# Kernel optimization log

Hardware: AMD Instinct MI355X
Metric: run time of the kernel (lower is better)

The kernel has to match this reference:

```python
import jax, jax.numpy as jnp
import numpy as np

B, S, D, H, FACTOR = 1, 2048, 1024, 16, 16
HD = D // H


def setup_inputs() -> dict:
    key = jax.random.key(0)
    ks = jax.random.split(key, 9)
    s = 1.0 / np.sqrt(D)
    u = lambda k, shape: jax.random.uniform(k, shape, jnp.float32, -s, s)
    return {
        "x": jax.random.normal(ks[0], (B, S, D), jnp.float32),
        "Wq": u(ks[1], (D, D)), "bq": u(ks[2], (D,)),
        "Wk": u(ks[3], (D, D)), "bk": u(ks[4], (D,)),
        "Wv": u(ks[5], (D, D)), "bv": u(ks[6], (D,)),
        "Wo": u(ks[7], (D, D)), "bo": u(ks[8], (D,)),
    }


def reference(x, Wq, bq, Wk, bk, Wv, bv, Wo, bo):
    b, s, d = x.shape
    h, hd = H, HD
    # projections -> [b, h, s, hd]
    q = (x @ Wq + bq).reshape(b, s, h, hd).transpose(0, 2, 1, 3)
    k = (x @ Wk + bk).reshape(b, s, h, hd).transpose(0, 2, 1, 3)
    v = (x @ Wv + bv).reshape(b, s, h, hd).transpose(0, 2, 1, 3)
    # dense scores [b, h, s, s]
    scores = jnp.einsum('bhqd,bhkd->bhqk', q, k) / np.sqrt(hd).astype(np.float32)
    # top-k along last dim, scatter into zeros (non-topk entries stay 0, as in torch code)
    vals, idx = jax.lax.top_k(scores, FACTOR)  # [b,h,s,FACTOR]
    flat_scores = scores.reshape(-1, s)
    rows = jnp.arange(flat_scores.shape[0])[:, None]
    sparse = jnp.zeros_like(flat_scores).at[rows, idx.reshape(-1, FACTOR)].set(
        vals.reshape(-1, FACTOR)).reshape(scores.shape)
    attn = jax.nn.softmax(sparse, axis=-1)  # softmax over sparse scores incl. zeros
    out = jnp.einsum('bhqk,bhkd->bhqd', attn, v)
    out = out.transpose(0, 2, 1, 3).reshape(b, s, d)
    return out @ Wo + bo
```

## Files before the change

kernel.cpp:

```cpp
#include <hip/hip_runtime.h>
#include <stdint.h>

constexpr int SEQ  = 2048;
constexpr int DIM  = 1024;
constexpr int NH   = 16;
constexpr int HDIM = 64;
constexpr int TOPK = 16;
constexpr int CAP  = 96;
constexpr int CST  = 97;
constexpr int QR   = 32;

typedef unsigned short bf16_t;
typedef __attribute__((ext_vector_type(8))) short bf16x8;
typedef __attribute__((ext_vector_type(4))) float f32x4;
typedef unsigned long long u64;

__device__ __forceinline__ int swzc(int col, int row) { return col ^ ((row & 7) << 3); }

__device__ __forceinline__ float bf2f(bf16_t b) {
  return __uint_as_float(((unsigned)b) << 16);
}
__device__ __forceinline__ bf16_t f2bf(float f) {
  unsigned u = __float_as_uint(f);
  unsigned r = u + 0x7fffu + ((u >> 16) & 1u);
  return (bf16_t)(r >> 16);
}
__device__ __forceinline__ f32x4 zero4() {
  f32x4 z; z[0] = 0.f; z[1] = 0.f; z[2] = 0.f; z[3] = 0.f; return z;
}
__device__ __forceinline__ void gload_lds16(const bf16_t* g, bf16_t* l) {
  __builtin_amdgcn_global_load_lds(
      (const __attribute__((address_space(1))) void*)g,
      (__attribute__((address_space(3))) void*)l, 16, 0, 0);
}
__device__ __forceinline__ unsigned ordf(float f) {
  unsigned b = __float_as_uint(f);
  return (b & 0x80000000u) ? ~b : (b | 0x80000000u);
}
__device__ __forceinline__ float iordf(unsigned u) {
  unsigned b = (u & 0x80000000u) ? (u ^ 0x80000000u) : ~u;
  return __uint_as_float(b);
}

__global__ void prep_kernel(const float* __restrict__ x, bf16_t* __restrict__ xb,
                            const float* __restrict__ W0, const float* __restrict__ W1,
                            const float* __restrict__ W2, const float* __restrict__ W3,
                            bf16_t* __restrict__ T0, bf16_t* __restrict__ T1,
                            bf16_t* __restrict__ T2, bf16_t* __restrict__ T3) {
  const int z = blockIdx.z;
  if (z == 4) {
    int bl = blockIdx.y * 32 + blockIdx.x;
    int tt = threadIdx.y * 32 + threadIdx.x;
    int i = (bl * 256 + tt) * 8;
    float4 v0 = *reinterpret_cast<const float4*>(x + i);
    float4 v1 = *reinterpret_cast<const float4*>(x + i + 4);
    bf16x8 o;
    o[0] = (short)f2bf(v0.x); o[1] = (short)f2bf(v0.y);
    o[2] = (short)f2bf(v0.z); o[3] = (short)f2bf(v0.w);
    o[4] = (short)f2bf(v1.x); o[5] = (short)f2bf(v1.y);
    o[6] = (short)f2bf(v1.z); o[7] = (short)f2bf(v1.w);
    *reinterpret_cast<bf16x8*>(xb + i) = o;
    return;
  }
  const float* W = (z == 0) ? W0 : (z == 1) ? W1 : (z == 2) ? W2 : W3;
  bf16_t* WT = (z == 0) ? T0 : (z == 1) ? T1 : (z == 2) ? T2 : T3;
  __shared__ float tile[32][33];
  int tx = threadIdx.x, ty = threadIdx.y;
  int bx = blockIdx.x * 32, by = blockIdx.y * 32;
#pragma unroll
  for (int i = 0; i < 4; ++i)
    tile[ty + i * 8][tx] = W[(by + ty + i * 8) * DIM + bx + tx];
  __syncthreads();
#pragma unroll
  for (int i = 0; i < 4; ++i)
    WT[(bx + ty + i * 8) * DIM + by + tx] = f2bf(tile[tx][ty + i * 8]);
}

template <int MODE>
__global__ __launch_bounds__(256) void gemm_t(const bf16_t* __restrict__ A,
                                              const bf16_t* __restrict__ B0,
                                              const bf16_t* __restrict__ B1,
                                              const bf16_t* __restrict__ B2,
                                              const float* __restrict__ c0,
                                              const float* __restrict__ c1,
                                              const float* __restrict__ c2,
                                              void* __restrict__ o0,
                                              void* __restrict__ o1,
                                              void* __restrict__ o2,
                                              float* __restrict__ sumv) {
  __shared__ __align__(16) bf16_t As[2][128 * 64];
  __shared__ __align__(16) bf16_t Bs[2][128 * 64];
  const int t = threadIdx.x;
  int which, bn0, ks0, nst;
  if (MODE == 0) {
    which = blockIdx.x >> 3; bn0 = (blockIdx.x & 7) * 128; ks0 = 0; nst = 16;
  } else {
    which = 0; bn0 = blockIdx.x * 128; ks0 = blockIdx.z * 8; nst = 8;
  }
  const bf16_t* Bt = (which == 0) ? B0 : (which == 1) ? B1 : B2;
  const float* bias = (which == 0) ? c0 : (which == 1) ? c1 : c2;
  void* out = (which == 0) ? o0 : (which == 1) ? o1 : o2;
  const int bm0 = blockIdx.y * 128;
  const int w = t >> 6, lane = t & 63, lr = lane & 15, lg = lane >> 4;
  const int wm = w >> 1, wn = w & 1;
  const int srow = t >> 3;
  const int scol = swzc((t & 7) * 8, srow);
  const int ldst = srow * 64 + (t & 7) * 8;
  const int rsw = (lr & 7) << 3;

  f32x4 acc[4][4];
#pragma unroll
  for (int m = 0; m < 4; ++m)
#pragma unroll
    for (int n = 0; n < 4; ++n) acc[m][n] = zero4();

#define STAGE_G(buf, kt)                                                             \
  do {                                                                               \
    _Pragma("unroll") for (int i_ = 0; i_ < 4; ++i_) {                               \
      gload_lds16(A + (size_t)(bm0 + i_ * 32 + srow) * DIM + (kt) * 64 + scol,       \
                  &As[buf][i_ * 32 * 64 + ldst]);                                    \
      gload_lds16(Bt + (size_t)(bn0 + i_ * 32 + srow) * DIM + (kt) * 64 + scol,      \
                  &Bs[buf][i_ * 32 * 64 + ldst]);                                    \
    }                                                                                \
  } while (0)

  STAGE_G(0, ks0);
  __syncthreads();

  for (int s = 0; s < nst; ++s) {
    const int cur = s & 1;
    if (s < nst - 1) STAGE_G(cur ^ 1, ks0 + s + 1);
    bf16x8 a[4][2], b[4][2];
#pragma unroll
    for (int m = 0; m < 4; ++m)
#pragma unroll
      for (int kk = 0; kk < 2; ++kk)
        a[m][kk] = *reinterpret_cast<const bf16x8*>(
            &As[cur][(wm * 64 + m * 16 + lr) * 64 + ((kk * 32 + lg * 8) ^ rsw)]);
#pragma unroll
    for (int n = 0; n < 4; ++n)
#pragma unroll
      for (int kk = 0; kk < 2; ++kk)
        b[n][kk] = *reinterpret_cast<const bf16x8*>(
            &Bs[cur][(wn * 64 + n * 16 + lr) * 64 + ((kk * 32 + lg * 8) ^ rsw)]);
#pragma unroll
    for (int m = 0; m < 4; ++m)
#pragma unroll
      for (int n = 0; n < 4; ++n)
#pragma unroll
        for (int kk = 0; kk < 2; ++kk)
          acc[m][n] = __builtin_amdgcn_mfma_f32_16x16x32_bf16(a[m][kk], b[n][kk],
                                                              acc[m][n], 0, 0, 0);
    __syncthreads();
  }
#undef STAGE_G

#pragma unroll
  for (int n = 0; n < 4; ++n) {
    int col = bn0 + wn * 64 + n * 16 + lr;
    float bv = bias[col];
    if (MODE == 0) {
      float colsum = 0.f;
#pragma unroll
      for (int m = 0; m < 4; ++m)
#pragma unroll
        for (int r = 0; r < 4; ++r) {
          int row = bm0 + wm * 64 + m * 16 + lg * 4 + r;
          bf16_t rb = f2bf(acc[m][n][r] + bv);
          reinterpret_cast<bf16_t*>(out)[(size_t)row * DIM + col] = rb;
          if (which == 2) colsum += bf2f(rb);
        }
      if (which == 2) atomicAdd(&sumv[col], colsum);
    } else {
      float badd = (ks0 == 0) ? bv : 0.f;
#pragma unroll
      for (int m = 0; m < 4; ++m)
#pragma unroll
        for (int r = 0; r < 4; ++r) {
          int row = bm0 + wm * 64 + m * 16 + lg * 4 + r;
          atomicAdd(reinterpret_cast<float*>(out) + (size_t)row * DIM + col,
                    acc[m][n][r] + badd);
        }
    }
  }
}

#define LOADK(buf, kc)                                                              \
  do {                                                                              \
    _Pragma("unroll") for (int n_ = 0; n_ < 4; ++n_)                                \
      _Pragma("unroll") for (int k_ = 0; k_ < 2; ++k_)                              \
        kf[buf][n_][k_] = *reinterpret_cast<const bf16x8*>(                         \
            kp + (size_t)((kc) * 64 + n_ * 16 + lr) * DIM + k_ * 32 + lg * 8);      \
  } while (0)

__global__ __launch_bounds__(256, 4) void attn_kernel(const bf16_t* __restrict__ q,
                                                      const bf16_t* __restrict__ k,
                                                      const bf16_t* __restrict__ v,
                                                      const float* __restrict__ sumv,
                                                      bf16_t* __restrict__ op) {
  __shared__ float CM[QR * 33];
  __shared__ float Tsh[QR];
  __shared__ float zsh[QR];
  __shared__ int   cnt[QR];
  __shared__ float cval[QR * CST];
  __shared__ unsigned short cidx[QR * CST];

  const int t = threadIdx.x;
  const int lin = blockIdx.x;
  const int xcd = lin & 7, ixd = lin >> 3;
  const int h = xcd * 2 + (ixd >> 6), qt = ixd & 63;
  const int w = t >> 6, lane = t & 63, lr = lane & 15, lg = lane >> 4;

  const bf16_t* qp = q + (size_t)(qt * QR) * DIM + h * HDIM;
  const bf16_t* kp = k + h * HDIM;

  bf16x8 aq[2][2];
#pragma unroll
  for (int m = 0; m < 2; ++m)
#pragma unroll
    for (int kk = 0; kk < 2; ++kk)
      aq[m][kk] = *reinterpret_cast<const bf16x8*>(
          qp + (size_t)(m * 16 + lr) * DIM + kk * 32 + lg * 8);

  bf16x8 kf[2][4][2];

  LOADK(0, w * 8);
#pragma unroll
  for (int i = 0; i < 8; ++i) {
    if (i < 7) LOADK((i + 1) & 1, w * 8 + i + 1);
    const int cur = i & 1;
    f32x4 sacc[2][4];
#pragma unroll
    for (int m = 0; m < 2; ++m)
#pragma unroll
      for (int n = 0; n < 4; ++n) sacc[m][n] = zero4();
#pragma unroll
    for (int m = 0; m < 2; ++m)
#pragma unroll
      for (int n = 0; n < 4; ++n)
#pragma unroll
        for (int kk = 0; kk < 2; ++kk)
          sacc[m][n] = __builtin_amdgcn_mfma_f32_16x16x32_bf16(kf[cur][n][kk], aq[m][kk],
                                                               sacc[m][n], 0, 0, 0);
#pragma unroll
    for (int m = 0; m < 2; ++m) {
      float mx = sacc[m][0][0];
#pragma unroll
      for (int n = 0; n < 4; ++n)
#pragma unroll
        for (int r = 0; r < 4; ++r) mx = fmaxf(mx, sacc[m][n][r]);
      mx = fmaxf(mx, __shfl_xor(mx, 16));
      mx = fmaxf(mx, __shfl_xor(mx, 32));
      if (lane < 16) CM[(m * 16 + lane) * 33 + (w * 8 + i)] = mx * 0.125f;
    }
  }
  LOADK(0, w * 8);
  __syncthreads();

  {
    const int trow = t >> 3, tsub = t & 7;
    float cmv[4];
#pragma unroll
    for (int c = 0; c < 4; ++c) cmv[c] = CM[trow * 33 + tsub * 4 + c];
    float Tval = -1e30f;
#pragma unroll
    for (int it = 0; it < TOPK; ++it) {
      float lm = fmaxf(fmaxf(cmv[0], cmv[1]), fmaxf(cmv[2], cmv[3]));
      float gm = fmaxf(lm, __shfl_xor(lm, 1));
      gm = fmaxf(gm, __shfl_xor(gm, 2));
      gm = fmaxf(gm, __shfl_xor(gm, 4));
      u64 b = __ballot(lm == gm);
      int base = lane & ~7;
      int ownsub = __ffsll((b >> base) & 0xFFull) - 1;
      if (tsub == ownsub) {
        bool d = false;
#pragma unroll
        for (int c = 0; c < 4; ++c)
          if (!d && cmv[c] == lm) { cmv[c] = -1e30f; d = true; }
      }
      Tval = gm;
    }
    if (tsub == 0) { Tsh[trow] = Tval; cnt[trow] = 0; }
  }
  __syncthreads();

  float Treg[2];
#pragma unroll
  for (int m = 0; m < 2; ++m) Treg[m] = Tsh[m * 16 + lr];

#pragma unroll
  for (int i = 0; i < 8; ++i) {
    if (i < 7) LOADK((i + 1) & 1, w * 8 + i + 1);
    const int cur = i & 1;
    const int kc = w * 8 + i;
    f32x4 sacc[2][4];
#pragma unroll
    for (int m = 0; m < 2; ++m)
#pragma unroll
      for (int n = 0; n < 4; ++n) sacc[m][n] = zero4();
#pragma unroll
    for (int m = 0; m < 2; ++m)
#pragma unroll
      for (int n = 0; n < 4; ++n)
#pragma unroll
        for (int kk = 0; kk < 2; ++kk)
          sacc[m][n] = __builtin_amdgcn_mfma_f32_16x16x32_bf16(kf[cur][n][kk], aq[m][kk],
                                                               sacc[m][n], 0, 0, 0);
#pragma unroll
    for (int m = 0; m < 2; ++m)
#pragma unroll
      for (int n = 0; n < 4; ++n)
#pragma unroll
        for (int r = 0; r < 4; ++r) {
          float val = sacc[m][n][r] * 0.125f;
          if (val >= Treg[m]) {
            int row = m * 16 + lr;
            int p = atomicAdd(&cnt[row], 1);
            if (p < CAP) {
              cval[row * CST + p] = val;
              cidx[row * CST + p] = (unsigned short)(kc * 64 + n * 16 + lg * 4 + r);
            }
          }
        }
  }
  __syncthreads();

  {
    const int trow = t >> 3, tsub = t & 7;
    int nc = cnt[trow]; if (nc > CAP) nc = CAP;
    float Zexp = 0.f;
    for (int sel = 0; sel < TOPK; ++sel) {
      u64 lmax = 0ull; int lp = -1;
      for (int p = tsub; p < nc; p += 8) {
        float vv = cval[trow * CST + p];
        unsigned id = cidx[trow * CST + p];
        u64 key = ((u64)ordf(vv) << 32) | (u64)(unsigned)(~id);
        if (key > lmax) { lmax = key; lp = p; }
      }
      u64 g = lmax;
#pragma unroll
      for (int d = 1; d < 8; d <<= 1) {
        u64 o = __shfl_xor(g, d);
        g = (o > g) ? o : g;
      }
      if (lmax == g && lp >= 0) cval[trow * CST + lp] = -1e30f;
      float val = iordf((unsigned)(g >> 32));
      int idx = (int)(~(unsigned)(g & 0xffffffffull));
      float e = expf(val);
      Zexp += e;
      if (tsub == 0) {
        CM[trow * 33 + sel] = e - 1.f;
        CM[trow * 33 + 16 + sel] = __int_as_float(idx);
      }
    }
    if (tsub == 0) zsh[trow] = 2032.f + Zexp;
  }
  __syncthreads();

  {
    const int row = t >> 3;
    const int dbase = h * HDIM + (t & 7) * 8;
    float oacc[8];
    const float4* sp = reinterpret_cast<const float4*>(sumv + dbase);
    float4 s0 = sp[0], s1 = sp[1];
    oacc[0] = s0.x; oacc[1] = s0.y; oacc[2] = s0.z; oacc[3] = s0.w;
    oacc[4] = s1.x; oacc[5] = s1.y; oacc[6] = s1.z; oacc[7] = s1.w;
    float invZ = 1.f / zsh[row];
#pragma unroll
    for (int j = 0; j < TOPK; ++j) {
      float wj = CM[row * 33 + j];
      int kidx = __float_as_int(CM[row * 33 + 16 + j]);
      bf16x8 vv = *reinterpret_cast<const bf16x8*>(v + (size_t)kidx * DIM + dbase);
#pragma unroll
      for (int e = 0; e < 8; ++e) oacc[e] += wj * bf2f((bf16_t)vv[e]);
    }
    bf16x8 o0;
#pragma unroll
    for (int e = 0; e < 8; ++e) o0[e] = (short)f2bf(oacc[e] * invZ);
    *reinterpret_cast<bf16x8*>(op + (size_t)(qt * QR + row) * DIM + dbase) = o0;
  }
}

extern "C" void kernel_launch(void* const* d_in, const int* in_sizes, int n_in,
                              void* d_out, int out_size, void* d_ws, size_t ws_size,
                              hipStream_t stream) {
  const float* x  = (const float*)d_in[0];
  const float* Wq = (const float*)d_in[1];
  const float* bq = (const float*)d_in[2];
  const float* Wk = (const float*)d_in[3];
  const float* bk = (const float*)d_in[4];
  const float* Wv = (const float*)d_in[5];
  const float* bv = (const float*)d_in[6];
  const float* Wo = (const float*)d_in[7];
  const float* bo = (const float*)d_in[8];
  float* out = (float*)d_out;

  char* ws = (char*)d_ws;
  bf16_t* xb   = (bf16_t*)(ws + (size_t)(0)  * (1 << 20));
  bf16_t* WqT  = (bf16_t*)(ws + (size_t)(4)  * (1 << 20));
  bf16_t* WkT  = (bf16_t*)(ws + (size_t)(6)  * (1 << 20));
  bf16_t* WvT  = (bf16_t*)(ws + (size_t)(8)  * (1 << 20));
  bf16_t* WoT  = (bf16_t*)(ws + (size_t)(10) * (1 << 20));
  bf16_t* qb   = (bf16_t*)(ws + (size_t)(12) * (1 << 20));
  bf16_t* kb   = (bf16_t*)(ws + (size_t)(16) * (1 << 20));
  bf16_t* vb   = (bf16_t*)(ws + (size_t)(20) * (1 << 20));
  bf16_t* opb  = (bf16_t*)(ws + (size_t)(24) * (1 << 20));
  float*  sumv = (float*) (ws + (size_t)(28) * (1 << 20));

  prep_kernel<<<dim3(32, 32, 5), dim3(32, 8), 0, stream>>>(x, xb, Wq, Wk, Wv, Wo,
                                                           WqT, WkT, WvT, WoT);
  hipMemsetAsync(sumv, 0, DIM * sizeof(float), stream);
  hipMemsetAsync(out, 0, (size_t)SEQ * DIM * sizeof(float), stream);

  gemm_t<0><<<dim3(24, 16), 256, 0, stream>>>(xb, WqT, WkT, WvT, bq, bk, bv,
                                              (void*)qb, (void*)kb, (void*)vb, sumv);

  attn_kernel<<<1024, 256, 0, stream>>>(qb, kb, vb, sumv, opb);

  gemm_t<1><<<dim3(8, 16, 2), 256, 0, stream>>>(opb, WoT, WoT, WoT, bo, bo, bo,
                                                (void*)out, (void*)out, (void*)out, sumv);
}
```

Before: 255.3 us.

## Replace split-K atomic output GEMM with 128x64 tiled direct-store kernel

The output projection GEMM drops its split-K layout, which relied on float atomicAdd into a zeroed output. It now uses a dedicated kernel with 128x64 tiles and a 16x16 grid that covers the full K dimension and stores results directly, so the output memset and the atomics go away. The attention kernel's launch bounds change from 4 to 2 waves-per-EU minimum, which allows more registers but may lower occupancy. Each block now does more K iterations, and there are 256 blocks instead of the earlier 256 split-K blocks.

```diff
diff --git a/kernel.cpp b/kernel.cpp
--- a/kernel.cpp
+++ b/kernel.cpp
@@ -76,31 +76,25 @@
     WT[(bx + ty + i * 8) * DIM + by + tx] = f2bf(tile[tx][ty + i * 8]);
 }
 
-template <int MODE>
-__global__ __launch_bounds__(256) void gemm_t(const bf16_t* __restrict__ A,
-                                              const bf16_t* __restrict__ B0,
-                                              const bf16_t* __restrict__ B1,
-                                              const bf16_t* __restrict__ B2,
-                                              const float* __restrict__ c0,
-                                              const float* __restrict__ c1,
-                                              const float* __restrict__ c2,
-                                              void* __restrict__ o0,
-                                              void* __restrict__ o1,
-                                              void* __restrict__ o2,
-                                              float* __restrict__ sumv) {
+__global__ __launch_bounds__(256) void gemm_qkv(const bf16_t* __restrict__ A,
+                                                const bf16_t* __restrict__ B0,
+                                                const bf16_t* __restrict__ B1,
+                                                const bf16_t* __restrict__ B2,
+                                                const float* __restrict__ c0,
+                                                const float* __restrict__ c1,
+                                                const float* __restrict__ c2,
+                                                bf16_t* __restrict__ o0,
+                                                bf16_t* __restrict__ o1,
+                                                bf16_t* __restrict__ o2,
+                                                float* __restrict__ sumv) {
   __shared__ __align__(16) bf16_t As[2][128 * 64];
   __shared__ __align__(16) bf16_t Bs[2][128 * 64];
   const int t = threadIdx.x;
-  int which, bn0, ks0, nst;
-  if (MODE == 0) {
-    which = blockIdx.x >> 3; bn0 = (blockIdx.x & 7) * 128; ks0 = 0; nst = 16;
-  } else {
-    which = 0; bn0 = blockIdx.x * 128; ks0 = blockIdx.z * 8; nst = 8;
-  }
+  const int which = blockIdx.x >> 3;
   const bf16_t* Bt = (which == 0) ? B0 : (which == 1) ? B1 : B2;
   const float* bias = (which == 0) ? c0 : (which == 1) ? c1 : c2;
-  void* out = (which == 0) ? o0 : (which == 1) ? o1 : o2;
-  const int bm0 = blockIdx.y * 128;
+  bf16_t* out = (which == 0) ? o0 : (which == 1) ? o1 : o2;
+  const int bm0 = blockIdx.y * 128, bn0 = (blockIdx.x & 7) * 128;
   const int w = t >> 6, lane = t & 63, lr = lane & 15, lg = lane >> 4;
   const int wm = w >> 1, wn = w & 1;
   const int srow = t >> 3;
@@ -124,12 +118,12 @@
     }                                                                                \
   } while (0)
 
-  STAGE_G(0, ks0);
-  __syncthreads();
-
-  for (int s = 0; s < nst; ++s) {
+  STAGE_G(0, 0);
+  __syncthreads();
+
+  for (int s = 0; s < 16; ++s) {
     const int cur = s & 1;
-    if (s < nst - 1) STAGE_G(cur ^ 1, ks0 + s + 1);
+    if (s < 15) STAGE_G(cur ^ 1, s + 1);
     bf16x8 a[4][2], b[4][2];
 #pragma unroll
     for (int m = 0; m < 4; ++m)
@@ -159,29 +153,93 @@
   for (int n = 0; n < 4; ++n) {
     int col = bn0 + wn * 64 + n * 16 + lr;
     float bv = bias[col];
-    if (MODE == 0) {
-      float colsum = 0.f;
-#pragma unroll
-      for (int m = 0; m < 4; ++m)
-#pragma unroll
-        for (int r = 0; r < 4; ++r) {
-          int row = bm0 + wm * 64 + m * 16 + lg * 4 + r;
-          bf16_t rb = f2bf(acc[m][n][r] + bv);
-          reinterpret_cast<bf16_t*>(out)[(size_t)row * DIM + col] = rb;
-          if (which == 2) colsum += bf2f(rb);
-        }
-      if (which == 2) atomicAdd(&sumv[col], colsum);
-    } else {
-      float badd = (ks0 == 0) ? bv : 0.f;
-#pragma unroll
-      for (int m = 0; m < 4; ++m)
-#pragma unroll
-        for (int r = 0; r < 4; ++r) {
-          int row = bm0 + wm * 64 + m * 16 + lg * 4 + r;
-          atomicAdd(reinterpret_cast<float*>(out) + (size_t)row * DIM + col,
-                    acc[m][n][r] + badd);
-        }
-    }
+    float colsum = 0.f;
+#pragma unroll
+    for (int m = 0; m < 4; ++m)
+#pragma unroll
+      for (int r = 0; r < 4; ++r) {
+        int row = bm0 + wm * 64 + m * 16 + lg * 4 + r;
+        bf16_t rb = f2bf(acc[m][n][r] + bv);
+        out[(size_t)row * DIM + col] = rb;
+        if (which == 2) colsum += bf2f(rb);
+      }
+    if (which == 2) atomicAdd(&sumv[col], colsum);
+  }
+}
+
+__global__ __launch_bounds__(256) void gemm_wo(const bf16_t* __restrict__ A,
+                                               const bf16_t* __restrict__ Bt,
+                                               const float* __restrict__ bias,
+                                               float* __restrict__ out) {
+  __shared__ __align__(16) bf16_t As[2][128 * 64];
+  __shared__ __align__(16) bf16_t Bs[2][64 * 64];
+  const int t = threadIdx.x;
+  const int bm0 = blockIdx.y * 128, bn0 = blockIdx.x * 64;
+  const int w = t >> 6, lane = t & 63, lr = lane & 15, lg = lane >> 4;
+  const int wm = w >> 1, wn = w & 1;
+  const int srow = t >> 3;
+  const int scol = swzc((t & 7) * 8, srow);
+  const int ldst = srow * 64 + (t & 7) * 8;
+  const int rsw = (lr & 7) << 3;
+
+  f32x4 acc[4][2];
+#pragma unroll
+  for (int m = 0; m < 4; ++m)
+#pragma unroll
+    for (int n = 0; n < 2; ++n) acc[m][n] = zero4();
+
+#define STAGE_W(buf, kt)                                                             \
+  do {                                                                               \
+    _Pragma("unroll") for (int i_ = 0; i_ < 4; ++i_)                                 \
+      gload_lds16(A + (size_t)(bm0 + i_ * 32 + srow) * DIM + (kt) * 64 + scol,       \
+                  &As[buf][i_ * 32 * 64 + ldst]);                                    \
+    _Pragma("unroll") for (int i_ = 0; i_ < 2; ++i_)                                 \
+      gload_lds16(Bt + (size_t)(bn0 + i_ * 32 + srow) * DIM + (kt) * 64 + scol,      \
+                  &Bs[buf][i_ * 32 * 64 + ldst]);                                    \
+  } while (0)
+
+  STAGE_W(0, 0);
+  __syncthreads();
+
+  for (int s = 0; s < 16; ++s) {
+    const int cur = s & 1;
+    if (s < 15) STAGE_W(cur ^ 1, s + 1);
+    bf16x8 a[4][2], b[2][2];
+#pragma unroll
+    for (int m = 0; m < 4; ++m)
+#pragma unroll
+      for (int kk = 0; kk < 2; ++kk)
+        a[m][kk] = *reinterpret_cast<const bf16x8*>(
+            &As[cur][(wm * 64 + m * 16 + lr) * 64 + ((kk * 32 + lg * 8) ^ rsw)]);
+#pragma unroll
+    for (int n = 0; n < 2; ++n)
+#pragma unroll
+      for (int kk = 0; kk < 2; ++kk)
+        b[n][kk] = *reinterpret_cast<const bf16x8*>(
+            &Bs[cur][(wn * 32 + n * 16 + lr) * 64 + ((kk * 32 + lg * 8) ^ rsw)]);
+#pragma unroll
+    for (int m = 0; m < 4; ++m)
+#pragma unroll
+      for (int n = 0; n < 2; ++n)
+#pragma unroll
+        for (int kk = 0; kk < 2; ++kk)
+          acc[m][n] = __builtin_amdgcn_mfma_f32_16x16x32_bf16(a[m][kk], b[n][kk],
+                                                              acc[m][n], 0, 0, 0);
+    __syncthreads();
+  }
+#undef STAGE_W
+
+#pragma unroll
+  for (int n = 0; n < 2; ++n) {
+    int col = bn0 + wn * 32 + n * 16 + lr;
+    float bv = bias[col];
+#pragma unroll
+    for (int m = 0; m < 4; ++m)
+#pragma unroll
+      for (int r = 0; r < 4; ++r) {
+        int row = bm0 + wm * 64 + m * 16 + lg * 4 + r;
+        out[(size_t)row * DIM + col] = acc[m][n][r] + bv;
+      }
   }
 }
 
@@ -193,7 +251,7 @@
             kp + (size_t)((kc) * 64 + n_ * 16 + lr) * DIM + k_ * 32 + lg * 8);      \
   } while (0)
 
-__global__ __launch_bounds__(256, 4) void attn_kernel(const bf16_t* __restrict__ q,
+__global__ __launch_bounds__(256, 2) void attn_kernel(const bf16_t* __restrict__ q,
                                                       const bf16_t* __restrict__ k,
                                                       const bf16_t* __restrict__ v,
                                                       const float* __restrict__ sumv,
@@ -410,13 +468,11 @@
   prep_kernel<<<dim3(32, 32, 5), dim3(32, 8), 0, stream>>>(x, xb, Wq, Wk, Wv, Wo,
                                                            WqT, WkT, WvT, WoT);
   hipMemsetAsync(sumv, 0, DIM * sizeof(float), stream);
-  hipMemsetAsync(out, 0, (size_t)SEQ * DIM * sizeof(float), stream);
-
-  gemm_t<0><<<dim3(24, 16), 256, 0, stream>>>(xb, WqT, WkT, WvT, bq, bk, bv,
-                                              (void*)qb, (void*)kb, (void*)vb, sumv);
+
+  gemm_qkv<<<dim3(24, 16), 256, 0, stream>>>(xb, WqT, WkT, WvT, bq, bk, bv,
+                                             qb, kb, vb, sumv);
 
   attn_kernel<<<1024, 256, 0, stream>>>(qb, kb, vb, sumv, opb);
 
-  gemm_t<1><<<dim3(8, 16, 2), 256, 0, stream>>>(opb, WoT, WoT, WoT, bo, bo, bo,
-                                                (void*)out, (void*)out, (void*)out, sumv);
-}
+  gemm_wo<<<dim3(16, 16), 256, 0, stream>>>(opb, WoT, bo, out);
+}
```

Result: faster. 232.3 us (-9.0%).
